# Kernel tuning notes

Measured on AMD Instinct MI355X. Metric: run time of the kernel, lower is better.

## Reference

```python
import jax, jax.numpy as jnp
import numpy as np

N_ITEMS = 30000
N_USERS = 20000
N_NODES = N_ITEMS + N_USERS  # 50000
N_EDGES = 512000
D0, D1, D2 = 768, 128, 64
EPS = 1e-12  # torch F.normalize eps


def _xavier(key, shape):
    fan_in, fan_out = shape
    bound = np.sqrt(6.0 / (fan_in + fan_out)).astype(np.float32)
    return jax.random.uniform(key, shape, jnp.float32, -bound, bound)


def setup_inputs() -> dict:
    key = jax.random.key(0)
    ks = jax.random.split(key, 12)
    return {
        "item_embed": jax.random.normal(ks[0], (N_ITEMS, D0), jnp.float32) * 0.05,
        "user_embed": jax.random.normal(ks[1], (N_USERS, D0), jnp.float32) * 0.05,
        "W1_0": _xavier(ks[2], (D0, D1)),
        "b1_0": jnp.zeros((D1,), jnp.float32),
        "W2_0": _xavier(ks[3], (D0, D1)),
        "b2_0": jnp.zeros((D1,), jnp.float32),
        "W1_1": _xavier(ks[4], (D1, D2)),
        "b1_1": jnp.zeros((D2,), jnp.float32),
        "W2_1": _xavier(ks[5], (D1, D2)),
        "b2_1": jnp.zeros((D2,), jnp.float32),
        # normalized-Laplacian-like positive edge weights
        "edge_vals": jax.random.uniform(ks[6], (N_EDGES,), jnp.float32) * 0.1,
        "edge_rows": jax.random.randint(ks[7], (N_EDGES,), 0, N_NODES, jnp.int32),
        "edge_cols": jax.random.randint(ks[8], (N_EDGES,), 0, N_NODES, jnp.int32),
    }


def _ngcf_layer(ego, edge_vals, edge_rows, edge_cols, W1, b1, W2, b2):
    # side = A_in @ ego : gather source features, scale, segment-sum into rows
    msg = edge_vals[:, None] * ego[edge_cols]            # (E, d) gather
    side = jax.ops.segment_sum(msg, edge_rows, num_segments=N_NODES)
    side_plus_I = side + ego                             # (A + I) @ ego
    simple = side_plus_I @ W1 + b1                       # linear1
    interaction = (side * ego) @ W2 + b2                 # linear2 on Hadamard
    return jax.nn.leaky_relu(simple + interaction)       # dropout = eval/no-op


def reference(item_embed, user_embed, W1_0, b1_0, W2_0, b2_0,
              W1_1, b1_1, W2_1, b2_1, edge_vals, edge_rows, edge_cols):
    ego = jnp.concatenate([item_embed, user_embed], axis=0)  # (N, 768)
    all_embed = [ego]
    for (W1, b1, W2, b2) in ((W1_0, b1_0, W2_0, b2_0), (W1_1, b1_1, W2_1, b2_1)):
        ego = _ngcf_layer(ego, edge_vals, edge_rows, edge_cols, W1, b1, W2, b2)
        norm = jnp.maximum(jnp.linalg.norm(ego, axis=1, keepdims=True), EPS)
        all_embed.append(ego / norm)
    return jnp.concatenate(all_embed, axis=1)  # (N, 768+128+64)
```

## Files before the change

### kernel.cpp

```cpp
#include <hip/hip_runtime.h>
#include <stdint.h>

#define N_ITEMS 30000
#define N_USERS 20000
#define N_NODES 50000
#define N_EDGES 512000
#define D0 768
#define D1 128
#define D2 64
#define OSTRIDE 960

typedef short bf16x8 __attribute__((ext_vector_type(8)));
typedef float f32x4  __attribute__((ext_vector_type(4)));

__device__ __forceinline__ unsigned short f2bf(float x) {
    union { float f; uint32_t u; } v; v.f = x;
    uint32_t u = v.u;
    return (unsigned short)((u + 0x7FFF + ((u >> 16) & 1)) >> 16);
}

__global__ __launch_bounds__(256) void copy_ego0(const float* __restrict__ item,
                                                 const float* __restrict__ user,
                                                 float* __restrict__ out) {
    int idx = blockIdx.x * 256 + threadIdx.x;
    if (idx >= N_NODES * (D0 / 4)) return;
    int row = idx / (D0 / 4);
    int c4  = idx % (D0 / 4);
    const float4* src = (row < N_ITEMS)
        ? (const float4*)(item + (size_t)row * D0)
        : (const float4*)(user + (size_t)(row - N_ITEMS) * D0);
    float4 v = src[c4];
    *(float4*)(out + (size_t)row * OSTRIDE + c4 * 4) = v;
}

__global__ __launch_bounds__(256) void histogram_kernel(const int* __restrict__ rows,
                                                        int* __restrict__ counts) {
    int e = blockIdx.x * 256 + threadIdx.x;
    if (e < N_EDGES) atomicAdd(&counts[rows[e]], 1);
}

#define SCAN_THREADS 1024
__global__ __launch_bounds__(1024) void scan_kernel(const int* __restrict__ counts,
                                                    int* __restrict__ offsets,
                                                    int* __restrict__ cursors) {
    __shared__ int partials[SCAN_THREADS];
    const int CH = (N_NODES + SCAN_THREADS - 1) / SCAN_THREADS;
    int t = threadIdx.x;
    int base = t * CH;
    int sum = 0;
    for (int i = 0; i < CH; i++) {
        int idx = base + i;
        if (idx < N_NODES) sum += counts[idx];
    }
    partials[t] = sum;
    __syncthreads();
    for (int off = 1; off < SCAN_THREADS; off <<= 1) {
        int add = (t >= off) ? partials[t - off] : 0;
        __syncthreads();
        partials[t] += add;
        __syncthreads();
    }
    int run = (t == 0) ? 0 : partials[t - 1];
    for (int i = 0; i < CH; i++) {
        int idx = base + i;
        if (idx < N_NODES) {
            offsets[idx] = run;
            cursors[idx] = run;
            run += counts[idx];
        }
    }
    if (t == SCAN_THREADS - 1) offsets[N_NODES] = N_EDGES;
}

__global__ __launch_bounds__(256) void fill_kernel(const float* __restrict__ vals,
                                                   const int* __restrict__ rows,
                                                   const int* __restrict__ cols,
                                                   int* __restrict__ cursors,
                                                   float* __restrict__ svals,
                                                   int* __restrict__ scols) {
    int e = blockIdx.x * 256 + threadIdx.x;
    if (e >= N_EDGES) return;
    int pos = atomicAdd(&cursors[rows[e]], 1);
    svals[pos] = vals[e];
    scols[pos] = cols[e];
}

template <int K, int N>
__global__ __launch_bounds__(256) void prep_wb(const float* __restrict__ W,
                                               unsigned short* __restrict__ Wb) {
    constexpr int FR = (K / 32) * (N / 16);
    int tid = blockIdx.x * 256 + threadIdx.x;
    if (tid >= FR * 64) return;
    int frag = tid >> 6, lane = tid & 63;
    int kk = frag / (N / 16), nt = frag % (N / 16);
    int quad = lane >> 4, n = lane & 15;
    unsigned short tmp[8];
#pragma unroll
    for (int jj = 0; jj < 8; jj++) {
        int k = kk * 32 + quad * 8 + jj;
        tmp[jj] = f2bf(W[(size_t)k * N + nt * 16 + n]);
    }
#pragma unroll
    for (int jj = 0; jj < 8; jj++) Wb[(size_t)tid * 8 + jj] = tmp[jj];
}

template <int DIN, int DOUT>
__global__ __launch_bounds__(256) void fused_layer_mfma(
    const int*   __restrict__ offsets,
    const float* __restrict__ svals,
    const int*   __restrict__ scols,
    const float* __restrict__ ego, int ego_stride,
    const unsigned short* __restrict__ Wb1,
    const unsigned short* __restrict__ Wb2,
    const float* __restrict__ b1, const float* __restrict__ b2,
    float* __restrict__ out, int out_stride)
{
    constexpr int NPB = 16;
    constexpr int KK  = DIN / 32;
    constexpr int NT  = DOUT / 16;
    constexpr int NTW = NT / 4;
    constexpr int PAD = 8;
    constexpr int CPL = DIN / 64;
    __shared__ unsigned short s_sum [NPB][DIN + PAD];
    __shared__ unsigned short s_prod[NPB][DIN + PAD];

    const int t = threadIdx.x;
    const int w = t >> 6, l = t & 63;
    const int node_base = blockIdx.x * NPB;

    for (int nn = 0; nn < 4; nn++) {
        int n   = w * 4 + nn;
        int row = node_base + n;
        int beg = offsets[row], end = offsets[row + 1];
        float acc[CPL], eg[CPL];
#pragma unroll
        for (int c = 0; c < CPL; c++) {
            acc[c] = 0.f;
            eg[c]  = ego[(size_t)row * ego_stride + l + 64 * c];
        }
        int e = beg;
        for (; e + 1 < end; e += 2) {
            float v0 = svals[e],     v1 = svals[e + 1];
            const float* sp0 = ego + (size_t)scols[e]     * ego_stride;
            const float* sp1 = ego + (size_t)scols[e + 1] * ego_stride;
#pragma unroll
            for (int c = 0; c < CPL; c++) acc[c] = fmaf(v0, sp0[l + 64 * c], acc[c]);
#pragma unroll
            for (int c = 0; c < CPL; c++) acc[c] = fmaf(v1, sp1[l + 64 * c], acc[c]);
        }
        if (e < end) {
            float v0 = svals[e];
            const float* sp0 = ego + (size_t)scols[e] * ego_stride;
#pragma unroll
            for (int c = 0; c < CPL; c++) acc[c] = fmaf(v0, sp0[l + 64 * c], acc[c]);
        }
#pragma unroll
        for (int c = 0; c < CPL; c++) {
            float s = acc[c], e2 = eg[c];
            s_sum [n][l + 64 * c] = f2bf(s + e2);
            s_prod[n][l + 64 * c] = f2bf(s * e2);
        }
    }
    __syncthreads();

    const int m = l & 15, quad = l >> 4;
    f32x4 acc[NTW] = {};
    for (int kk = 0; kk < KK; kk++) {
        bf16x8 a_s = *(const bf16x8*)&s_sum [m][kk * 32 + quad * 8];
        bf16x8 a_p = *(const bf16x8*)&s_prod[m][kk * 32 + quad * 8];
#pragma unroll
        for (int i = 0; i < NTW; i++) {
            int nt = w * NTW + i;
            bf16x8 bf1 = *(const bf16x8*)(Wb1 + ((size_t)(kk * NT + nt) * 64 + l) * 8);
            bf16x8 bf2 = *(const bf16x8*)(Wb2 + ((size_t)(kk * NT + nt) * 64 + l) * 8);
            acc[i] = __builtin_amdgcn_mfma_f32_16x16x32_bf16(a_s, bf1, acc[i], 0, 0, 0);
            acc[i] = __builtin_amdgcn_mfma_f32_16x16x32_bf16(a_p, bf2, acc[i], 0, 0, 0);
        }
    }

#pragma unroll
    for (int i = 0; i < NTW; i++) {
        int nt = w * NTW + i;
        int j  = nt * 16 + m;
        float bb = b1[j] + b2[j];
#pragma unroll
        for (int r = 0; r < 4; r++) {
            int node  = node_base + quad * 4 + r;
            float val = acc[i][r] + bb;
            val = val > 0.f ? val : 0.01f * val;
            out[(size_t)node * out_stride + j] = val;
        }
    }
}

__global__ __launch_bounds__(64) void normalize_kernel(float* __restrict__ out) {
    int row  = blockIdx.x;
    int lane = threadIdx.x;
    float* p1 = out + (size_t)row * OSTRIDE + D0;
    float* p2 = p1 + D1;

    float2 v = *(float2*)(p1 + lane * 2);
    float ss = v.x * v.x + v.y * v.y;
#pragma unroll
    for (int off = 32; off > 0; off >>= 1) ss += __shfl_xor(ss, off, 64);
    float inv1 = 1.0f / fmaxf(sqrtf(ss), 1e-12f);
    v.x *= inv1; v.y *= inv1;
    *(float2*)(p1 + lane * 2) = v;

    float wv = p2[lane];
    float ss2 = wv * wv;
#pragma unroll
    for (int off = 32; off > 0; off >>= 1) ss2 += __shfl_xor(ss2, off, 64);
    p2[lane] = wv / fmaxf(sqrtf(ss2), 1e-12f);
}

extern "C" void kernel_launch(void* const* d_in, const int* in_sizes, int n_in,
                              void* d_out, int out_size, void* d_ws, size_t ws_size,
                              hipStream_t stream) {
    const float* item  = (const float*)d_in[0];
    const float* user  = (const float*)d_in[1];
    const float* W1_0  = (const float*)d_in[2];
    const float* b1_0  = (const float*)d_in[3];
    const float* W2_0  = (const float*)d_in[4];
    const float* b2_0  = (const float*)d_in[5];
    const float* W1_1  = (const float*)d_in[6];
    const float* b1_1  = (const float*)d_in[7];
    const float* W2_1  = (const float*)d_in[8];
    const float* b2_1  = (const float*)d_in[9];
    const float* evals = (const float*)d_in[10];
    const int*   erows = (const int*)d_in[11];
    const int*   ecols = (const int*)d_in[12];
    float* out = (float*)d_out;

    int*   counts  = (int*)d_ws;
    int*   offsets = counts + N_NODES;
    int*   cursors = offsets + (N_NODES + 1);
    float* svals   = (float*)((int*)d_ws + 150004);
    int*   scols   = (int*)(svals + N_EDGES);
    unsigned short* wb1_0 = (unsigned short*)(scols + N_EDGES);
    unsigned short* wb2_0 = wb1_0 + (size_t)D0 * D1;
    unsigned short* wb1_1 = wb2_0 + (size_t)D0 * D1;
    unsigned short* wb2_1 = wb1_1 + (size_t)D1 * D2;

    copy_ego0<<<(N_NODES * (D0 / 4) + 255) / 256, 256, 0, stream>>>(item, user, out);

    hipMemsetAsync(counts, 0, (size_t)N_NODES * sizeof(int), stream);
    histogram_kernel<<<(N_EDGES + 255) / 256, 256, 0, stream>>>(erows, counts);
    scan_kernel<<<1, SCAN_THREADS, 0, stream>>>(counts, offsets, cursors);
    fill_kernel<<<(N_EDGES + 255) / 256, 256, 0, stream>>>(evals, erows, ecols,
                                                           cursors, svals, scols);

    {
        constexpr int FR0 = (D0 / 32) * (D1 / 16);
        constexpr int FR1 = (D1 / 32) * (D2 / 16);
        prep_wb<D0, D1><<<(FR0 * 64 + 255) / 256, 256, 0, stream>>>(W1_0, wb1_0);
        prep_wb<D0, D1><<<(FR0 * 64 + 255) / 256, 256, 0, stream>>>(W2_0, wb2_0);
        prep_wb<D1, D2><<<(FR1 * 64 + 255) / 256, 256, 0, stream>>>(W1_1, wb1_1);
        prep_wb<D1, D2><<<(FR1 * 64 + 255) / 256, 256, 0, stream>>>(W2_1, wb2_1);
    }

    fused_layer_mfma<D0, D1><<<N_NODES / 16, 256, 0, stream>>>(
        offsets, svals, scols, out, OSTRIDE,
        wb1_0, wb2_0, b1_0, b2_0, out + D0, OSTRIDE);

    fused_layer_mfma<D1, D2><<<N_NODES / 16, 256, 0, stream>>>(
        offsets, svals, scols, out + D0, OSTRIDE,
        wb1_1, wb2_1, b1_1, b2_1, out + D0 + D1, OSTRIDE);

    normalize_kernel<<<N_NODES, 64, 0, stream>>>(out);
}
```

Baseline: 812.9 us.

## Gather neighbor features from bf16 copies with vectorized loads and wider blocks

```diff
diff --git a/kernel.cpp b/kernel.cpp
--- a/kernel.cpp
+++ b/kernel.cpp
@@ -12,16 +12,22 @@
 
 typedef short bf16x8 __attribute__((ext_vector_type(8)));
 typedef float f32x4  __attribute__((ext_vector_type(4)));
+typedef unsigned short u16x4 __attribute__((ext_vector_type(4)));
+typedef unsigned short u16x2 __attribute__((ext_vector_type(2)));
 
 __device__ __forceinline__ unsigned short f2bf(float x) {
     union { float f; uint32_t u; } v; v.f = x;
     uint32_t u = v.u;
     return (unsigned short)((u + 0x7FFF + ((u >> 16) & 1)) >> 16);
 }
+__device__ __forceinline__ float bf2f(unsigned short s) {
+    union { uint32_t u; float f; } v; v.u = ((uint32_t)s) << 16; return v.f;
+}
 
 __global__ __launch_bounds__(256) void copy_ego0(const float* __restrict__ item,
                                                  const float* __restrict__ user,
-                                                 float* __restrict__ out) {
+                                                 float* __restrict__ out,
+                                                 unsigned short* __restrict__ outb) {
     int idx = blockIdx.x * 256 + threadIdx.x;
     if (idx >= N_NODES * (D0 / 4)) return;
     int row = idx / (D0 / 4);
@@ -31,6 +37,11 @@
         : (const float4*)(user + (size_t)(row - N_ITEMS) * D0);
     float4 v = src[c4];
     *(float4*)(out + (size_t)row * OSTRIDE + c4 * 4) = v;
+    if (outb) {
+        u16x4 b;
+        b[0] = f2bf(v.x); b[1] = f2bf(v.y); b[2] = f2bf(v.z); b[3] = f2bf(v.w);
+        *(u16x4*)(outb + (size_t)row * D0 + c4 * 4) = b;
+    }
 }
 
 __global__ __launch_bounds__(256) void histogram_kernel(const int* __restrict__ rows,
@@ -104,23 +115,29 @@
     for (int jj = 0; jj < 8; jj++) Wb[(size_t)tid * 8 + jj] = tmp[jj];
 }
 
-template <int DIN, int DOUT>
-__global__ __launch_bounds__(256) void fused_layer_mfma(
+template <int DIN, int DOUT, int THREADS, bool BSRC>
+__global__ __launch_bounds__(THREADS) void fused_layer_mfma(
     const int*   __restrict__ offsets,
     const float* __restrict__ svals,
     const int*   __restrict__ scols,
     const float* __restrict__ ego, int ego_stride,
+    const unsigned short* __restrict__ egob,
     const unsigned short* __restrict__ Wb1,
     const unsigned short* __restrict__ Wb2,
     const float* __restrict__ b1, const float* __restrict__ b2,
-    float* __restrict__ out, int out_stride)
+    float* __restrict__ out, int out_stride,
+    unsigned short* __restrict__ outb)
 {
-    constexpr int NPB = 16;
-    constexpr int KK  = DIN / 32;
-    constexpr int NT  = DOUT / 16;
-    constexpr int NTW = NT / 4;
-    constexpr int PAD = 8;
-    constexpr int CPL = DIN / 64;
+    constexpr int NPB   = 16;
+    constexpr int WAVES = THREADS / 64;
+    constexpr int NPW   = NPB / WAVES;
+    constexpr int KK    = DIN / 32;
+    constexpr int NT    = DOUT / 16;
+    constexpr int NTW   = NT / WAVES;
+    constexpr int PAD   = 8;
+    constexpr int CW    = (DIN >= 256) ? 4 : 2;
+    constexpr int NC    = DIN / (64 * CW);
+
     __shared__ unsigned short s_sum [NPB][DIN + PAD];
     __shared__ unsigned short s_prod[NPB][DIN + PAD];
 
@@ -128,43 +145,92 @@
     const int w = t >> 6, l = t & 63;
     const int node_base = blockIdx.x * NPB;
 
-    for (int nn = 0; nn < 4; nn++) {
-        int n   = w * 4 + nn;
+    for (int nn = 0; nn < NPW; nn++) {
+        int n   = w * NPW + nn;
         int row = node_base + n;
         int beg = offsets[row], end = offsets[row + 1];
-        float acc[CPL], eg[CPL];
-#pragma unroll
-        for (int c = 0; c < CPL; c++) {
-            acc[c] = 0.f;
-            eg[c]  = ego[(size_t)row * ego_stride + l + 64 * c];
-        }
-        int e = beg;
-        for (; e + 1 < end; e += 2) {
-            float v0 = svals[e],     v1 = svals[e + 1];
-            const float* sp0 = ego + (size_t)scols[e]     * ego_stride;
-            const float* sp1 = ego + (size_t)scols[e + 1] * ego_stride;
-#pragma unroll
-            for (int c = 0; c < CPL; c++) acc[c] = fmaf(v0, sp0[l + 64 * c], acc[c]);
-#pragma unroll
-            for (int c = 0; c < CPL; c++) acc[c] = fmaf(v1, sp1[l + 64 * c], acc[c]);
-        }
-        if (e < end) {
-            float v0 = svals[e];
-            const float* sp0 = ego + (size_t)scols[e] * ego_stride;
-#pragma unroll
-            for (int c = 0; c < CPL; c++) acc[c] = fmaf(v0, sp0[l + 64 * c], acc[c]);
-        }
-#pragma unroll
-        for (int c = 0; c < CPL; c++) {
-            float s = acc[c], e2 = eg[c];
-            s_sum [n][l + 64 * c] = f2bf(s + e2);
-            s_prod[n][l + 64 * c] = f2bf(s * e2);
+        float acc[NC * CW];
+#pragma unroll
+        for (int c = 0; c < NC * CW; c++) acc[c] = 0.f;
+
+        auto gather_one = [&](int gc, float v) {
+            if constexpr (BSRC) {
+                const unsigned short* sp = egob + (size_t)gc * DIN;
+#pragma unroll
+                for (int c = 0; c < NC; c++) {
+                    if constexpr (CW == 4) {
+                        u16x4 q = *(const u16x4*)(sp + c * 256 + l * 4);
+#pragma unroll
+                        for (int j = 0; j < 4; j++)
+                            acc[c * 4 + j] = fmaf(v, bf2f(q[j]), acc[c * 4 + j]);
+                    } else {
+                        u16x2 q = *(const u16x2*)(sp + l * 2);
+                        acc[0] = fmaf(v, bf2f(q[0]), acc[0]);
+                        acc[1] = fmaf(v, bf2f(q[1]), acc[1]);
+                    }
+                }
+            } else {
+                const float* sp = ego + (size_t)gc * ego_stride;
+#pragma unroll
+                for (int c = 0; c < NC; c++) {
+                    if constexpr (CW == 4) {
+                        float4 q = *(const float4*)(sp + c * 256 + l * 4);
+                        acc[c * 4 + 0] = fmaf(v, q.x, acc[c * 4 + 0]);
+                        acc[c * 4 + 1] = fmaf(v, q.y, acc[c * 4 + 1]);
+                        acc[c * 4 + 2] = fmaf(v, q.z, acc[c * 4 + 2]);
+                        acc[c * 4 + 3] = fmaf(v, q.w, acc[c * 4 + 3]);
+                    } else {
+                        float2 q = *(const float2*)(sp + l * 2);
+                        acc[0] = fmaf(v, q.x, acc[0]);
+                        acc[1] = fmaf(v, q.y, acc[1]);
+                    }
+                }
+            }
+        };
+
+        for (int base = beg; base < end; base += 64) {
+            int cnt = min(64, end - base);
+            int   cl = 0;
+            float vl = 0.f;
+            if (l < cnt) { cl = scols[base + l]; vl = svals[base + l]; }
+            int u = 0;
+            for (; u + 1 < cnt; u += 2) {
+                int   g0 = __shfl(cl, u),     g1 = __shfl(cl, u + 1);
+                float v0 = __shfl(vl, u),     v1 = __shfl(vl, u + 1);
+                gather_one(g0, v0);
+                gather_one(g1, v1);
+            }
+            if (u < cnt) gather_one(__shfl(cl, u), __shfl(vl, u));
+        }
+
+#pragma unroll
+        for (int c = 0; c < NC; c++) {
+            if constexpr (CW == 4) {
+                float4 e4 = *(const float4*)(ego + (size_t)row * ego_stride + c * 256 + l * 4);
+                float eg[4] = {e4.x, e4.y, e4.z, e4.w};
+                u16x4 s, p;
+#pragma unroll
+                for (int j = 0; j < 4; j++) {
+                    float a = acc[c * 4 + j];
+                    s[j] = f2bf(a + eg[j]);
+                    p[j] = f2bf(a * eg[j]);
+                }
+                *(u16x4*)&s_sum [n][c * 256 + l * 4] = s;
+                *(u16x4*)&s_prod[n][c * 256 + l * 4] = p;
+            } else {
+                float2 e2 = *(const float2*)(ego + (size_t)row * ego_stride + l * 2);
+                u16x2 s, p;
+                s[0] = f2bf(acc[0] + e2.x); p[0] = f2bf(acc[0] * e2.x);
+                s[1] = f2bf(acc[1] + e2.y); p[1] = f2bf(acc[1] * e2.y);
+                *(u16x2*)&s_sum [n][l * 2] = s;
+                *(u16x2*)&s_prod[n][l * 2] = p;
+            }
         }
     }
     __syncthreads();
 
     const int m = l & 15, quad = l >> 4;
-    f32x4 acc[NTW] = {};
+    f32x4 accc[NTW] = {};
     for (int kk = 0; kk < KK; kk++) {
         bf16x8 a_s = *(const bf16x8*)&s_sum [m][kk * 32 + quad * 8];
         bf16x8 a_p = *(const bf16x8*)&s_prod[m][kk * 32 + quad * 8];
@@ -173,8 +239,8 @@
             int nt = w * NTW + i;
             bf16x8 bf1 = *(const bf16x8*)(Wb1 + ((size_t)(kk * NT + nt) * 64 + l) * 8);
             bf16x8 bf2 = *(const bf16x8*)(Wb2 + ((size_t)(kk * NT + nt) * 64 + l) * 8);
-            acc[i] = __builtin_amdgcn_mfma_f32_16x16x32_bf16(a_s, bf1, acc[i], 0, 0, 0);
-            acc[i] = __builtin_amdgcn_mfma_f32_16x16x32_bf16(a_p, bf2, acc[i], 0, 0, 0);
+            accc[i] = __builtin_amdgcn_mfma_f32_16x16x32_bf16(a_s, bf1, accc[i], 0, 0, 0);
+            accc[i] = __builtin_amdgcn_mfma_f32_16x16x32_bf16(a_p, bf2, accc[i], 0, 0, 0);
         }
     }
 
@@ -186,9 +252,10 @@
 #pragma unroll
         for (int r = 0; r < 4; r++) {
             int node  = node_base + quad * 4 + r;
-            float val = acc[i][r] + bb;
+            float val = accc[i][r] + bb;
             val = val > 0.f ? val : 0.01f * val;
             out[(size_t)node * out_stride + j] = val;
+            if (outb) outb[(size_t)node * DOUT + j] = f2bf(val);
         }
     }
 }
@@ -241,8 +308,14 @@
     unsigned short* wb2_0 = wb1_0 + (size_t)D0 * D1;
     unsigned short* wb1_1 = wb2_0 + (size_t)D0 * D1;
     unsigned short* wb2_1 = wb1_1 + (size_t)D1 * D2;
-
-    copy_ego0<<<(N_NODES * (D0 / 4) + 255) / 256, 256, 0, stream>>>(item, user, out);
+    unsigned short* ego0b = wb2_1 + (size_t)D1 * D2;
+    unsigned short* ego1b = ego0b + (size_t)N_NODES * D0;
+
+    const size_t need = 5122000 + (size_t)N_NODES * D0 * 2 + (size_t)N_NODES * D1 * 2;
+    const bool big = ws_size >= need;
+
+    copy_ego0<<<(N_NODES * (D0 / 4) + 255) / 256, 256, 0, stream>>>(
+        item, user, out, big ? ego0b : nullptr);
 
     hipMemsetAsync(counts, 0, (size_t)N_NODES * sizeof(int), stream);
     histogram_kernel<<<(N_EDGES + 255) / 256, 256, 0, stream>>>(erows, counts);
@@ -259,13 +332,21 @@
         prep_wb<D1, D2><<<(FR1 * 64 + 255) / 256, 256, 0, stream>>>(W2_1, wb2_1);
     }
 
-    fused_layer_mfma<D0, D1><<<N_NODES / 16, 256, 0, stream>>>(
-        offsets, svals, scols, out, OSTRIDE,
-        wb1_0, wb2_0, b1_0, b2_0, out + D0, OSTRIDE);
-
-    fused_layer_mfma<D1, D2><<<N_NODES / 16, 256, 0, stream>>>(
-        offsets, svals, scols, out + D0, OSTRIDE,
-        wb1_1, wb2_1, b1_1, b2_1, out + D0 + D1, OSTRIDE);
+    if (big) {
+        fused_layer_mfma<D0, D1, 512, true><<<N_NODES / 16, 512, 0, stream>>>(
+            offsets, svals, scols, out, OSTRIDE, ego0b,
+            wb1_0, wb2_0, b1_0, b2_0, out + D0, OSTRIDE, ego1b);
+        fused_layer_mfma<D1, D2, 256, true><<<N_NODES / 16, 256, 0, stream>>>(
+            offsets, svals, scols, out + D0, OSTRIDE, ego1b,
+            wb1_1, wb2_1, b1_1, b2_1, out + D0 + D1, OSTRIDE, nullptr);
+    } else {
+        fused_layer_mfma<D0, D1, 512, false><<<N_NODES / 16, 512, 0, stream>>>(
+            offsets, svals, scols, out, OSTRIDE, nullptr,
+            wb1_0, wb2_0, b1_0, b2_0, out + D0, OSTRIDE, nullptr);
+        fused_layer_mfma<D1, D2, 256, false><<<N_NODES / 16, 256, 0, stream>>>(
+            offsets, svals, scols, out + D0, OSTRIDE, nullptr,
+            wb1_1, wb2_1, b1_1, b2_1, out + D0 + D1, OSTRIDE, nullptr);
+    }
 
     normalize_kernel<<<N_NODES, 64, 0, stream>>>(out);
 }
```

Result: faster. 718.2 us (-11.6%).
